# Optimization experiments

Hardware: AMD Instinct MI355X
Metric: run time of the kernel (lower is better)

## Reference

```python
import jax, jax.numpy as jnp
import numpy as np

B, S, E = 16, 2048, 1024

def setup_inputs() -> dict:
    key = jax.random.key(0)
    ks = jax.random.split(key, 7)
    scale = 1.0 / np.sqrt(E)
    x = jax.random.normal(ks[0], (B, S, E), dtype=jnp.float32)
    wq = jax.random.normal(ks[1], (E, E), dtype=jnp.float32) * scale
    bq = jax.random.normal(ks[2], (E,), dtype=jnp.float32) * 0.01
    wk = jax.random.normal(ks[3], (E, E), dtype=jnp.float32) * scale
    bk = jax.random.normal(ks[4], (E,), dtype=jnp.float32) * 0.01
    wv = jax.random.normal(ks[5], (E, E), dtype=jnp.float32) * scale
    bv = jax.random.normal(ks[6], (E,), dtype=jnp.float32) * 0.01
    return {"x": x, "wq": wq, "bq": bq, "wk": wk, "bk": bk, "wv": wv, "bv": bv}

def reference(x, wq, bq, wk, bk, wv, bv):
    # Linear layers: y = x @ W^T + b (torch nn.Linear convention)
    Q = jnp.einsum('bse,fe->bsf', x, wq) + bq
    K = jnp.einsum('bse,fe->bsf', x, wk) + bk
    V = jnp.einsum('bse,fe->bsf', x, wv) + bv
    scale = 1.0 / jnp.sqrt(jnp.asarray(x.shape[-1], dtype=x.dtype))
    score = jnp.einsum('bqe,bke->bqk', Q, K) * scale  # [B,S,S]
    attn = jax.nn.softmax(score, axis=-1)
    # dropout is identity in eval mode
    context = jnp.einsum('bqk,bke->bqe', attn, V)  # [B,S,E]
    return jnp.mean(context, axis=1)  # [B,E]
```

## Files before the change

kernel.cpp:

```cpp
#include <hip/hip_runtime.h>


#define B_ 16
#define S_ 2048
#define E_ 1024

typedef __bf16 bf16x8 __attribute__((ext_vector_type(8)));
typedef float f32x4 __attribute__((ext_vector_type(4)));
typedef float f32x2 __attribute__((ext_vector_type(2)));

__device__ __forceinline__ unsigned short f2bf(float f) {
  unsigned int u = __float_as_uint(f);
  u = (u + 0x7FFFu + ((u >> 16) & 1u)) >> 16;
  return (unsigned short)u;
}

__global__ __launch_bounds__(256) void gvec_kernel(
    const float* __restrict__ wk, const float* __restrict__ bq,
    float* __restrict__ g) {
  const int e = blockIdx.x * 256 + threadIdx.x;
  const int f0 = blockIdx.y * 32;
  float acc = 0.f;
#pragma unroll
  for (int i = 0; i < 32; ++i) acc += wk[(size_t)(f0 + i) * E_ + e] * bq[f0 + i];
  atomicAdd(&g[e], acc);
}

__global__ __launch_bounds__(256) void cast_x_v_kernel(
    const float* __restrict__ x, const float* __restrict__ g,
    unsigned short* __restrict__ xbf, float* __restrict__ vs) {
  const int row = blockIdx.x, t = threadIdx.x;
  const size_t i = (size_t)row * E_ + t * 4;
  float4 v = *(const float4*)(x + i);
  float4 gv = *(const float4*)(g + t * 4);
  ushort4 o;
  o.x = f2bf(v.x); o.y = f2bf(v.y); o.z = f2bf(v.z); o.w = f2bf(v.w);
  *(ushort4*)(xbf + i) = o;
  float p = v.x * gv.x + v.y * gv.y + v.z * gv.z + v.w * gv.w;
#pragma unroll
  for (int off = 32; off >= 1; off >>= 1) p += __shfl_xor(p, off);
  __shared__ float wsp[4];
  if ((t & 63) == 0) wsp[t >> 6] = p;
  __syncthreads();
  if (t == 0) vs[row] = (wsp[0] + wsp[1] + wsp[2] + wsp[3]) * 0.03125f;
}

__global__ __launch_bounds__(256) void tcast_kernel(
    const float* __restrict__ src, unsigned short* __restrict__ dst) {
  __shared__ float tile[32][33];
  const int tx = threadIdx.x & 31, ty = threadIdx.x >> 5;
  const int f0 = blockIdx.y * 32, e0 = blockIdx.x * 32;
#pragma unroll
  for (int j = 0; j < 4; ++j)
    tile[ty + 8 * j][tx] = src[(size_t)(f0 + ty + 8 * j) * E_ + e0 + tx];
  __syncthreads();
#pragma unroll
  for (int j = 0; j < 4; ++j)
    dst[(size_t)(e0 + ty + 8 * j) * E_ + f0 + tx] = f2bf(tile[tx][ty + 8 * j]);
}

template <int MODE>
__global__ __launch_bounds__(256, 2) void gemm_bt(
    const unsigned short* __restrict__ A, const unsigned short* __restrict__ Bm,
    void* __restrict__ Cout, const float* __restrict__ vs,
    float* __restrict__ rowsum, float scale,
    int K, int lda, int ldb, int ldc,
    long long strideA, long long strideB, long long strideC) {
  __shared__ unsigned short As[128 * 64];
  __shared__ unsigned short Bs[128 * 64];

  const int tid = threadIdx.x;
  const int wave = tid >> 6;
  const int lane = tid & 63;
  const int bz = blockIdx.z;
  const unsigned short* Ab = A + (size_t)bz * strideA;
  const unsigned short* Bb = Bm + (size_t)bz * strideB;
  const int rowBase = blockIdx.y * 128;
  const int colBase = blockIdx.x * 128;

  const int waveM = wave >> 1, waveN = wave & 1;
  const int lrow = lane & 15, lq = lane >> 4;

  const int rsub = lane >> 3;
  const int gOff = (((lane & 7) ^ rsub) << 3);

  f32x4 acc[4][4];
#pragma unroll
  for (int i = 0; i < 4; ++i)
#pragma unroll
    for (int j = 0; j < 4; ++j) {
      f32x4 z = {0.f, 0.f, 0.f, 0.f};
      acc[i][j] = z;
    }

  for (int k0 = 0; k0 < K; k0 += 64) {
#pragma unroll
    for (int i = 0; i < 4; ++i) {
      const int chunk = wave * 4 + i;
      const int r = chunk * 8 + rsub;
      const unsigned short* ga = Ab + (size_t)(rowBase + r) * lda + (k0 + gOff);
      const unsigned short* gb = Bb + (size_t)(colBase + r) * ldb + (k0 + gOff);
      __builtin_amdgcn_global_load_lds(
          (const __attribute__((address_space(1))) void*)ga,
          (__attribute__((address_space(3))) void*)(&As[chunk * 512]), 16, 0, 0);
      __builtin_amdgcn_global_load_lds(
          (const __attribute__((address_space(1))) void*)gb,
          (__attribute__((address_space(3))) void*)(&Bs[chunk * 512]), 16, 0, 0);
    }
    __syncthreads();

#pragma unroll
    for (int ks = 0; ks < 2; ++ks) {
      const int gg = (((ks * 4 + lq) ^ (lrow & 7)) << 3);
      bf16x8 af[4], bfv[4];
#pragma unroll
      for (int mi = 0; mi < 4; ++mi)
        af[mi] = *(const bf16x8*)(&As[(waveM * 64 + mi * 16 + lrow) * 64 + gg]);
#pragma unroll
      for (int ni = 0; ni < 4; ++ni)
        bfv[ni] = *(const bf16x8*)(&Bs[(waveN * 64 + ni * 16 + lrow) * 64 + gg]);
#pragma unroll
      for (int mi = 0; mi < 4; ++mi)
#pragma unroll
        for (int ni = 0; ni < 4; ++ni)
          acc[mi][ni] = __builtin_amdgcn_mfma_f32_16x16x32_bf16(
              af[mi], bfv[ni], acc[mi][ni], 0, 0, 0);
    }
    __syncthreads();
  }

  if constexpr (MODE == 0) {
    unsigned short* Cb = (unsigned short*)Cout;
#pragma unroll
    for (int mi = 0; mi < 4; ++mi) {
      const int grow = rowBase + waveM * 64 + mi * 16 + lq * 4;
#pragma unroll
      for (int ni = 0; ni < 4; ++ni) {
        const int gcol = colBase + waveN * 64 + ni * 16 + lrow;
#pragma unroll
        for (int r = 0; r < 4; ++r)
          Cb[(size_t)(grow + r) * ldc + gcol] = f2bf(acc[mi][ni][r]);
      }
    }
  }
}

template <int MODE>
__global__ __launch_bounds__(512, 2) void gemm256(
    const unsigned short* __restrict__ A, const unsigned short* __restrict__ Bm,
    void* __restrict__ Cout, const float* __restrict__ vs,
    float* __restrict__ rowsum, float scale, int ldc,
    long long strideA, long long strideB, long long strideC) {
  extern __shared__ __align__(16) unsigned short lds[];
  const int tid = threadIdx.x;
  const int wave = tid >> 6;
  const int lane = tid & 63;
  const int waveM = wave >> 2, waveN = wave & 3;
  const int lrow = lane & 15, lq = lane >> 4;
  const int bz = blockIdx.z;
  const int rowBase = blockIdx.y * 256;
  const int colBase = blockIdx.x * 256;
  const unsigned short* Ab = A + (size_t)bz * strideA;
  const unsigned short* Bb = Bm + (size_t)bz * strideB;

  const int rsub = lane >> 3;
  const int gsw = ((lane & 7) ^ rsub) << 3;
  const unsigned short* Ag =
      Ab + (size_t)(rowBase + wave * 8 + rsub) * E_ + gsw;
  const unsigned short* Bg =
      Bb + (size_t)(colBase + (wave >> 2) * 64 + (wave & 3) * 8 + rsub) * E_ + gsw;
  const int ALo = wave * 512;
  const int BLo = (wave >> 2) * 4096 + (wave & 3) * 512;

#define STG(gp, lo)                                             \
  __builtin_amdgcn_global_load_lds(                             \
      (const __attribute__((address_space(1))) void*)(gp),      \
      (__attribute__((address_space(3))) void*)(lds + (lo)), 16, 0, 0)
#define STG_A0(ko, q)                                   \
  do {                                                  \
    STG(Ag + (ko), (q) * 16384 + ALo);                  \
    STG(Ag + (ko) + 131072, (q) * 16384 + ALo + 8192);  \
  } while (0)
#define STG_A1(ko, q)                                   \
  do {                                                  \
    STG(Ag + (ko) + 65536, (q) * 16384 + ALo + 4096);   \
    STG(Ag + (ko) + 196608, (q) * 16384 + ALo + 12288); \
  } while (0)
#define STG_B0(ko, q)                                            \
  do {                                                           \
    STG(Bg + (ko), 32768 + (q) * 16384 + BLo);                   \
    STG(Bg + (ko) + 131072, 32768 + (q) * 16384 + BLo + 8192);   \
  } while (0)
#define STG_B1(ko, q)                                            \
  do {                                                           \
    STG(Bg + (ko) + 32768, 32768 + (q) * 16384 + BLo + 2048);    \
    STG(Bg + (ko) + 163840, 32768 + (q) * 16384 + BLo + 10240);  \
  } while (0)

  f32x4 acc[8][4];
#pragma unroll
  for (int i = 0; i < 8; ++i)
#pragma unroll
    for (int j = 0; j < 4; ++j) {
      f32x4 z = {0.f, 0.f, 0.f, 0.f};
      acc[i][j] = z;
    }

  STG_A0(0, 0); STG_B0(0, 0); STG_B1(0, 0); STG_A1(0, 0);
  STG_A0(64, 1); STG_B0(64, 1); STG_B1(64, 1); STG_A1(64, 1);
  asm volatile("s_waitcnt vmcnt(8)" ::: "memory");
  __builtin_amdgcn_s_barrier();

  const int rowA = (waveM * 128 + lrow) * 64;
  const int rowB = (waveN * 64 + lrow) * 64;
  const int g0 = (lq ^ (lrow & 7)) * 8;
  const int g1 = ((4 | lq) ^ (lrow & 7)) * 8;

  bf16x8 a[4][2], b0[2][2], b1[2][2];

#pragma unroll 2
  for (int t = 0; t < 16; ++t) {
    const int q = t & 1;
    const unsigned short* At = lds + q * 16384;
    const unsigned short* Bt = lds + 32768 + q * 16384;
    const int ko = t * 64 + 128;
    const bool st = (t < 14);

#pragma unroll
    for (int mi = 0; mi < 4; ++mi) {
      a[mi][0] = *(const bf16x8*)(At + rowA + mi * 1024 + g0);
      a[mi][1] = *(const bf16x8*)(At + rowA + mi * 1024 + g1);
    }
#pragma unroll
    for (int ni = 0; ni < 2; ++ni) {
      b0[ni][0] = *(const bf16x8*)(Bt + rowB + ni * 1024 + g0);
      b0[ni][1] = *(const bf16x8*)(Bt + rowB + ni * 1024 + g1);
    }
    __builtin_amdgcn_s_barrier();
    asm volatile("s_waitcnt lgkmcnt(0)" ::: "memory");
    __builtin_amdgcn_s_setprio(1);
#pragma unroll
    for (int mi = 0; mi < 4; ++mi)
#pragma unroll
      for (int ni = 0; ni < 2; ++ni) {
        acc[mi][ni] = __builtin_amdgcn_mfma_f32_16x16x32_bf16(
            a[mi][0], b0[ni][0], acc[mi][ni], 0, 0, 0);
        acc[mi][ni] = __builtin_amdgcn_mfma_f32_16x16x32_bf16(
            a[mi][1], b0[ni][1], acc[mi][ni], 0, 0, 0);
      }
    __builtin_amdgcn_s_setprio(0);
    __builtin_amdgcn_s_barrier();

#pragma unroll
    for (int ni = 0; ni < 2; ++ni) {
      b1[ni][0] = *(const bf16x8*)(Bt + rowB + (ni + 2) * 1024 + g0);
      b1[ni][1] = *(const bf16x8*)(Bt + rowB + (ni + 2) * 1024 + g1);
    }
    if (st) STG_A0(ko, q);
    __builtin_amdgcn_s_barrier();
    asm volatile("s_waitcnt lgkmcnt(0)" ::: "memory");
    __builtin_amdgcn_s_setprio(1);
#pragma unroll
    for (int mi = 0; mi < 4; ++mi)
#pragma unroll
      for (int ni = 0; ni < 2; ++ni) {
        acc[mi][ni + 2] = __builtin_amdgcn_mfma_f32_16x16x32_bf16(
            a[mi][0], b1[ni][0], acc[mi][ni + 2], 0, 0, 0);
        acc[mi][ni + 2] = __builtin_amdgcn_mfma_f32_16x16x32_bf16(
            a[mi][1], b1[ni][1], acc[mi][ni + 2], 0, 0, 0);
      }
    __builtin_amdgcn_s_setprio(0);
    __builtin_amdgcn_s_barrier();

#pragma unroll
    for (int mi = 0; mi < 4; ++mi) {
      a[mi][0] = *(const bf16x8*)(At + rowA + (mi + 4) * 1024 + g0);
      a[mi][1] = *(const bf16x8*)(At + rowA + (mi + 4) * 1024 + g1);
    }
    if (st) STG_B0(ko, q);
    __builtin_amdgcn_s_barrier();
    asm volatile("s_waitcnt lgkmcnt(0)" ::: "memory");
    __builtin_amdgcn_s_setprio(1);
#pragma unroll
    for (int mi = 0; mi < 4; ++mi)
#pragma unroll
      for (int ni = 0; ni < 2; ++ni) {
        acc[mi + 4][ni + 2] = __builtin_amdgcn_mfma_f32_16x16x32_bf16(
            a[mi][0], b1[ni][0], acc[mi + 4][ni + 2], 0, 0, 0);
        acc[mi + 4][ni + 2] = __builtin_amdgcn_mfma_f32_16x16x32_bf16(
            a[mi][1], b1[ni][1], acc[mi + 4][ni + 2], 0, 0, 0);
      }
    __builtin_amdgcn_s_setprio(0);
    __builtin_amdgcn_s_barrier();

    if (st) { STG_B1(ko, q); STG_A1(ko, q); }
    __builtin_amdgcn_s_barrier();
    __builtin_amdgcn_s_setprio(1);
#pragma unroll
    for (int mi = 0; mi < 4; ++mi)
#pragma unroll
      for (int ni = 0; ni < 2; ++ni) {
        acc[mi + 4][ni] = __builtin_amdgcn_mfma_f32_16x16x32_bf16(
            a[mi][0], b0[ni][0], acc[mi + 4][ni], 0, 0, 0);
        acc[mi + 4][ni] = __builtin_amdgcn_mfma_f32_16x16x32_bf16(
            a[mi][1], b0[ni][1], acc[mi + 4][ni], 0, 0, 0);
      }
    __builtin_amdgcn_s_setprio(0);
    if (st)
      asm volatile("s_waitcnt vmcnt(8)" ::: "memory");
    else
      asm volatile("s_waitcnt vmcnt(0)" ::: "memory");
    __builtin_amdgcn_s_barrier();
  }
#undef STG_B1
#undef STG_B0
#undef STG_A1
#undef STG_A0
#undef STG

  if constexpr (MODE == 0) {
    unsigned short* Cb = (unsigned short*)Cout;
#pragma unroll
    for (int mi = 0; mi < 8; ++mi) {
      const int grow = rowBase + waveM * 128 + mi * 16 + lq * 4;
#pragma unroll
      for (int ni = 0; ni < 4; ++ni) {
        const int gcol = colBase + waveN * 64 + ni * 16 + lrow;
#pragma unroll
        for (int r = 0; r < 4; ++r)
          Cb[(size_t)(grow + r) * ldc + gcol] = f2bf(acc[mi][ni][r]);
      }
    }
  } else {
    unsigned char* Eb = (unsigned char*)Cout + (size_t)bz * strideC;
    float* rs = rowsum + (size_t)bz * S_;
    const float* vsb = vs + (size_t)bz * S_;
    float badd[4];
#pragma unroll
    for (int ni = 0; ni < 4; ++ni)
      badd[ni] = vsb[colBase + waveN * 64 + ni * 16 + lrow];
#pragma unroll
    for (int mi = 0; mi < 8; ++mi) {
      const int grow = rowBase + waveM * 128 + mi * 16 + lq * 4;
#pragma unroll
      for (int r = 0; r < 4; ++r) {
        float e[4];
        float partial = 0.f;
#pragma unroll
        for (int ni = 0; ni < 4; ++ni) {
          e[ni] = __expf(acc[mi][ni][r] * scale + badd[ni]);
          partial += e[ni];
        }
        unsigned int pk = 0;
        pk = __builtin_amdgcn_cvt_pk_fp8_f32(e[0], e[1], pk, false);
        pk = __builtin_amdgcn_cvt_pk_fp8_f32(e[2], e[3], pk, true);
        *(unsigned int*)(&Eb[(size_t)(grow + r) * S_ + colBase + waveN * 64 +
                             lrow * 4]) = pk;
        partial += __shfl_xor(partial, 1);
        partial += __shfl_xor(partial, 2);
        partial += __shfl_xor(partial, 4);
        partial += __shfl_xor(partial, 8);
        if (lrow == 0) atomicAdd(&rs[grow + r], partial);
      }
    }
  }
}

__global__ __launch_bounds__(256) void colsum_kernel(
    const unsigned int* __restrict__ Epk, const float* __restrict__ rowsum,
    float* __restrict__ wsum) {
  const int b = blockIdx.y, q0 = blockIdx.x * 64, t = threadIdx.x;
  __shared__ float rinv[64];
  if (t < 64) rinv[t] = 1.0f / rowsum[(size_t)b * S_ + q0 + t];
  __syncthreads();
  float cs[2][4] = {{0, 0, 0, 0}, {0, 0, 0, 0}};
  const unsigned int* Eb = Epk + ((size_t)b * S_ + q0) * (S_ / 4);
  for (int q = 0; q < 64; ++q) {
    const float rv = rinv[q];
    const unsigned int* row = Eb + (size_t)q * (S_ / 4);
#pragma unroll
    for (int j = 0; j < 2; ++j) {
      const unsigned int p = row[t + 256 * j];
      f32x2 lo = __builtin_amdgcn_cvt_pk_f32_fp8(p, false);
      f32x2 hi = __builtin_amdgcn_cvt_pk_f32_fp8(p, true);
      cs[j][0] += lo[0] * rv;
      cs[j][1] += lo[1] * rv;
      cs[j][2] += hi[0] * rv;
      cs[j][3] += hi[1] * rv;
    }
  }
  const float inv = 1.0f / (float)S_;
#pragma unroll
  for (int j = 0; j < 2; ++j) {
    const int d = t + 256 * j;
    const int base = (d >> 4) * 64 + (d & 15);
#pragma unroll
    for (int jj = 0; jj < 4; ++jj)
      atomicAdd(&wsum[(size_t)b * S_ + base + 16 * jj], cs[j][jj] * inv);
  }
}

__global__ __launch_bounds__(256) void xbar_kernel(
    const unsigned short* __restrict__ xbf, const float* __restrict__ wsum,
    float* __restrict__ xbar) {
  const int b = blockIdx.y, kc = blockIdx.x, t = threadIdx.x;
  float4 acc = {0.f, 0.f, 0.f, 0.f};
  for (int k0 = 0; k0 < 128; ++k0) {
    const int k = kc * 128 + k0;
    const float w = wsum[(size_t)b * S_ + k];
    const ushort4 xv =
        *(const ushort4*)(xbf + ((size_t)b * S_ + k) * E_ + t * 4);
    acc.x += w * __uint_as_float((unsigned int)xv.x << 16);
    acc.y += w * __uint_as_float((unsigned int)xv.y << 16);
    acc.z += w * __uint_as_float((unsigned int)xv.z << 16);
    acc.w += w * __uint_as_float((unsigned int)xv.w << 16);
  }
  float* xb = xbar + (size_t)b * E_ + t * 4;
  atomicAdd(&xb[0], acc.x);
  atomicAdd(&xb[1], acc.y);
  atomicAdd(&xb[2], acc.z);
  atomicAdd(&xb[3], acc.w);
}

__global__ __launch_bounds__(256) void out_kernel(
    const float* __restrict__ xbar, const float* __restrict__ wv,
    const float* __restrict__ bv, float* __restrict__ out) {
  const int gid = blockIdx.x * 256 + threadIdx.x;
  const int b = gid >> 10, e = gid & 1023;
  const int c0 = blockIdx.y * 64;
  const float4* xr = (const float4*)(xbar + (size_t)b * E_) + c0;
  const float4* wr = (const float4*)(wv + (size_t)e * E_) + c0;
  float s = 0.f;
  for (int j = 0; j < 64; ++j) {
    float4 a = xr[j], w = wr[j];
    s += a.x * w.x + a.y * w.y + a.z * w.z + a.w * w.w;
  }
  if (blockIdx.y == 0) s += bv[e];
  atomicAdd(&out[gid], s);
}

extern "C" void kernel_launch(void* const* d_in, const int* in_sizes, int n_in,
                              void* d_out, int out_size, void* d_ws,
                              size_t ws_size, hipStream_t stream) {
  const float* x = (const float*)d_in[0];
  const float* wq = (const float*)d_in[1];
  const float* bq = (const float*)d_in[2];
  const float* wk = (const float*)d_in[3];
  const float* wv = (const float*)d_in[5];
  const float* bv = (const float*)d_in[6];
  float* out = (float*)d_out;

  char* ws = (char*)d_ws;
  const size_t MB = 1ull << 20;
  unsigned short* xbf = (unsigned short*)(ws);
  unsigned short* y = (unsigned short*)(ws + 64 * MB);
  unsigned char* Ebuf = (unsigned char*)(ws + 128 * MB);
  unsigned short* WqT = (unsigned short*)(ws + 192 * MB);
  unsigned short* WkT = (unsigned short*)(ws + 194 * MB);
  unsigned short* Mt = (unsigned short*)(ws + 196 * MB);
  float* g = (float*)(ws + 198 * MB);
  float* rowsum = g + E_;
  float* wsum = rowsum + B_ * S_;
  float* xbar = wsum + B_ * S_;
  float* vs = xbar + B_ * E_;

  hipFuncSetAttribute(reinterpret_cast<const void*>(gemm256<0>),
                      hipFuncAttributeMaxDynamicSharedMemorySize, 131072);
  hipFuncSetAttribute(reinterpret_cast<const void*>(gemm256<1>),
                      hipFuncAttributeMaxDynamicSharedMemorySize, 131072);

  hipMemsetAsync(g, 0, (size_t)(E_ + 2 * B_ * S_ + B_ * E_) * sizeof(float),
                 stream);
  hipMemsetAsync(out, 0, (size_t)B_ * E_ * sizeof(float), stream);

  gvec_kernel<<<dim3(E_ / 256, 32), 256, 0, stream>>>(wk, bq, g);
  cast_x_v_kernel<<<B_ * S_, 256, 0, stream>>>(x, g, xbf, vs);
  tcast_kernel<<<dim3(32, 32), 256, 0, stream>>>(wq, WqT);
  tcast_kernel<<<dim3(32, 32), 256, 0, stream>>>(wk, WkT);

  gemm_bt<0><<<dim3(8, 8), 256, 0, stream>>>(
      WkT, WqT, (void*)Mt, nullptr, nullptr, 1.0f, E_, E_, E_, E_, 0, 0, 0);
  gemm256<0><<<dim3(E_ / 256, (B_ * S_) / 256), 512, 131072, stream>>>(
      xbf, Mt, (void*)y, nullptr, nullptr, 1.0f, E_, 0, 0, 0);
  gemm256<1><<<dim3(S_ / 256, S_ / 256, B_), 512, 131072, stream>>>(
      y, xbf, (void*)Ebuf, vs, rowsum, 0.03125f, S_,
      (long long)S_ * E_, (long long)S_ * E_, (long long)S_ * S_);

  colsum_kernel<<<dim3(S_ / 64, B_), 256, 0, stream>>>(
      (const unsigned int*)Ebuf, rowsum, wsum);
  xbar_kernel<<<dim3(16, B_), 256, 0, stream>>>(xbf, wsum, xbar);
  out_kernel<<<dim3(B_ * E_ / 256, 4), 256, 0, stream>>>(xbar, wv, bv, out);
}
```

Measured before the change: 480.0 us.

## Move score GEMM to 128-tile kernel and retune small reduction kernels

```diff
diff --git a/kernel.cpp b/kernel.cpp
--- a/kernel.cpp
+++ b/kernel.cpp
@@ -29,20 +29,26 @@
 __global__ __launch_bounds__(256) void cast_x_v_kernel(
     const float* __restrict__ x, const float* __restrict__ g,
     unsigned short* __restrict__ xbf, float* __restrict__ vs) {
-  const int row = blockIdx.x, t = threadIdx.x;
-  const size_t i = (size_t)row * E_ + t * 4;
-  float4 v = *(const float4*)(x + i);
-  float4 gv = *(const float4*)(g + t * 4);
-  ushort4 o;
-  o.x = f2bf(v.x); o.y = f2bf(v.y); o.z = f2bf(v.z); o.w = f2bf(v.w);
-  *(ushort4*)(xbf + i) = o;
-  float p = v.x * gv.x + v.y * gv.y + v.z * gv.z + v.w * gv.w;
+  const int t = threadIdx.x;
+  const int row = blockIdx.x * 4 + (t >> 6);
+  const int lane = t & 63;
+  const float4* xr = (const float4*)(x + (size_t)row * E_);
+  const float4* g4 = (const float4*)g;
+  ushort4* xb4 = (ushort4*)(xbf + (size_t)row * E_);
+  float p = 0.f;
+#pragma unroll
+  for (int j = 0; j < 4; ++j) {
+    const int idx = j * 64 + lane;
+    float4 v = xr[idx];
+    float4 gv = g4[idx];
+    ushort4 o;
+    o.x = f2bf(v.x); o.y = f2bf(v.y); o.z = f2bf(v.z); o.w = f2bf(v.w);
+    xb4[idx] = o;
+    p += v.x * gv.x + v.y * gv.y + v.z * gv.z + v.w * gv.w;
+  }
 #pragma unroll
   for (int off = 32; off >= 1; off >>= 1) p += __shfl_xor(p, off);
-  __shared__ float wsp[4];
-  if ((t & 63) == 0) wsp[t >> 6] = p;
-  __syncthreads();
-  if (t == 0) vs[row] = (wsp[0] + wsp[1] + wsp[2] + wsp[3]) * 0.03125f;
+  if (lane == 0) vs[row] = p * 0.03125f;
 }
 
 __global__ __launch_bounds__(256) void tcast_kernel(
@@ -140,6 +146,38 @@
 #pragma unroll
         for (int r = 0; r < 4; ++r)
           Cb[(size_t)(grow + r) * ldc + gcol] = f2bf(acc[mi][ni][r]);
+      }
+    }
+  } else {
+    unsigned char* Eb = (unsigned char*)Cout + (size_t)bz * strideC;
+    float* rs = rowsum + (size_t)bz * S_;
+    const float* vsb = vs + (size_t)bz * S_;
+    float badd[4];
+#pragma unroll
+    for (int ni = 0; ni < 4; ++ni)
+      badd[ni] = vsb[colBase + waveN * 64 + ni * 16 + lrow];
+#pragma unroll
+    for (int mi = 0; mi < 4; ++mi) {
+      const int grow = rowBase + waveM * 64 + mi * 16 + lq * 4;
+#pragma unroll
+      for (int r = 0; r < 4; ++r) {
+        float e[4];
+        float partial = 0.f;
+#pragma unroll
+        for (int ni = 0; ni < 4; ++ni) {
+          e[ni] = __expf(acc[mi][ni][r] * scale + badd[ni]);
+          partial += e[ni];
+        }
+        unsigned int pk = 0;
+        pk = __builtin_amdgcn_cvt_pk_fp8_f32(e[0], e[1], pk, false);
+        pk = __builtin_amdgcn_cvt_pk_fp8_f32(e[2], e[3], pk, true);
+        *(unsigned int*)(&Eb[(size_t)(grow + r) * S_ + colBase + waveN * 64 +
+                             lrow * 4]) = pk;
+        partial += __shfl_xor(partial, 1);
+        partial += __shfl_xor(partial, 2);
+        partial += __shfl_xor(partial, 4);
+        partial += __shfl_xor(partial, 8);
+        if (lrow == 0) atomicAdd(&rs[grow + r], partial);
       }
     }
   }
@@ -331,51 +369,20 @@
           Cb[(size_t)(grow + r) * ldc + gcol] = f2bf(acc[mi][ni][r]);
       }
     }
-  } else {
-    unsigned char* Eb = (unsigned char*)Cout + (size_t)bz * strideC;
-    float* rs = rowsum + (size_t)bz * S_;
-    const float* vsb = vs + (size_t)bz * S_;
-    float badd[4];
-#pragma unroll
-    for (int ni = 0; ni < 4; ++ni)
-      badd[ni] = vsb[colBase + waveN * 64 + ni * 16 + lrow];
-#pragma unroll
-    for (int mi = 0; mi < 8; ++mi) {
-      const int grow = rowBase + waveM * 128 + mi * 16 + lq * 4;
-#pragma unroll
-      for (int r = 0; r < 4; ++r) {
-        float e[4];
-        float partial = 0.f;
-#pragma unroll
-        for (int ni = 0; ni < 4; ++ni) {
-          e[ni] = __expf(acc[mi][ni][r] * scale + badd[ni]);
-          partial += e[ni];
-        }
-        unsigned int pk = 0;
-        pk = __builtin_amdgcn_cvt_pk_fp8_f32(e[0], e[1], pk, false);
-        pk = __builtin_amdgcn_cvt_pk_fp8_f32(e[2], e[3], pk, true);
-        *(unsigned int*)(&Eb[(size_t)(grow + r) * S_ + colBase + waveN * 64 +
-                             lrow * 4]) = pk;
-        partial += __shfl_xor(partial, 1);
-        partial += __shfl_xor(partial, 2);
-        partial += __shfl_xor(partial, 4);
-        partial += __shfl_xor(partial, 8);
-        if (lrow == 0) atomicAdd(&rs[grow + r], partial);
-      }
-    }
   }
 }
 
 __global__ __launch_bounds__(256) void colsum_kernel(
     const unsigned int* __restrict__ Epk, const float* __restrict__ rowsum,
     float* __restrict__ wsum) {
-  const int b = blockIdx.y, q0 = blockIdx.x * 64, t = threadIdx.x;
-  __shared__ float rinv[64];
-  if (t < 64) rinv[t] = 1.0f / rowsum[(size_t)b * S_ + q0 + t];
+  const int b = blockIdx.y, q0 = blockIdx.x * 32, t = threadIdx.x;
+  __shared__ float rinv[32];
+  if (t < 32) rinv[t] = 1.0f / rowsum[(size_t)b * S_ + q0 + t];
   __syncthreads();
   float cs[2][4] = {{0, 0, 0, 0}, {0, 0, 0, 0}};
   const unsigned int* Eb = Epk + ((size_t)b * S_ + q0) * (S_ / 4);
-  for (int q = 0; q < 64; ++q) {
+#pragma unroll 2
+  for (int q = 0; q < 32; ++q) {
     const float rv = rinv[q];
     const unsigned int* row = Eb + (size_t)q * (S_ / 4);
 #pragma unroll
@@ -405,8 +412,9 @@
     float* __restrict__ xbar) {
   const int b = blockIdx.y, kc = blockIdx.x, t = threadIdx.x;
   float4 acc = {0.f, 0.f, 0.f, 0.f};
-  for (int k0 = 0; k0 < 128; ++k0) {
-    const int k = kc * 128 + k0;
+#pragma unroll 4
+  for (int k0 = 0; k0 < 64; ++k0) {
+    const int k = kc * 64 + k0;
     const float w = wsum[(size_t)b * S_ + k];
     const ushort4 xv =
         *(const ushort4*)(xbf + ((size_t)b * S_ + k) * E_ + t * 4);
@@ -466,15 +474,13 @@
 
   hipFuncSetAttribute(reinterpret_cast<const void*>(gemm256<0>),
                       hipFuncAttributeMaxDynamicSharedMemorySize, 131072);
-  hipFuncSetAttribute(reinterpret_cast<const void*>(gemm256<1>),
-                      hipFuncAttributeMaxDynamicSharedMemorySize, 131072);
 
   hipMemsetAsync(g, 0, (size_t)(E_ + 2 * B_ * S_ + B_ * E_) * sizeof(float),
                  stream);
   hipMemsetAsync(out, 0, (size_t)B_ * E_ * sizeof(float), stream);
 
   gvec_kernel<<<dim3(E_ / 256, 32), 256, 0, stream>>>(wk, bq, g);
-  cast_x_v_kernel<<<B_ * S_, 256, 0, stream>>>(x, g, xbf, vs);
+  cast_x_v_kernel<<<B_ * S_ / 4, 256, 0, stream>>>(x, g, xbf, vs);
   tcast_kernel<<<dim3(32, 32), 256, 0, stream>>>(wq, WqT);
   tcast_kernel<<<dim3(32, 32), 256, 0, stream>>>(wk, WkT);
 
@@ -482,12 +488,12 @@
       WkT, WqT, (void*)Mt, nullptr, nullptr, 1.0f, E_, E_, E_, E_, 0, 0, 0);
   gemm256<0><<<dim3(E_ / 256, (B_ * S_) / 256), 512, 131072, stream>>>(
       xbf, Mt, (void*)y, nullptr, nullptr, 1.0f, E_, 0, 0, 0);
-  gemm256<1><<<dim3(S_ / 256, S_ / 256, B_), 512, 131072, stream>>>(
-      y, xbf, (void*)Ebuf, vs, rowsum, 0.03125f, S_,
+  gemm_bt<1><<<dim3(S_ / 128, S_ / 128, B_), 256, 0, stream>>>(
+      y, xbf, (void*)Ebuf, vs, rowsum, 0.03125f, E_, E_, E_, S_,
       (long long)S_ * E_, (long long)S_ * E_, (long long)S_ * S_);
 
-  colsum_kernel<<<dim3(S_ / 64, B_), 256, 0, stream>>>(
+  colsum_kernel<<<dim3(S_ / 32, B_), 256, 0, stream>>>(
       (const unsigned int*)Ebuf, rowsum, wsum);
-  xbar_kernel<<<dim3(16, B_), 256, 0, stream>>>(xbf, wsum, xbar);
+  xbar_kernel<<<dim3(32, B_), 256, 0, stream>>>(xbf, wsum, xbar);
   out_kernel<<<dim3(B_ * E_ / 256, 4), 256, 0, stream>>>(xbar, wv, bv, out);
 }
```

After: 482.8 us. No clear change (+0.6%).
